# Optimization experiments

Measured on AMD Instinct MI355X. Metric: run time of the kernel, lower is better.

Reference implementation:

```python
import jax, jax.numpy as jnp
import numpy as np

EPS_FP32 = 1e-8
MASK_VALUE = -1.0e9
D_MODEL = 1024
N_HEADS = 16
D_K = D_MODEL // N_HEADS
SCALE = 1.0 / np.sqrt(D_K)


def stable_softmax(x, axis=-1):
    x_max = jnp.max(x, axis=axis, keepdims=True)
    e = jnp.exp(x - x_max)
    return e / (jnp.sum(e, axis=axis, keepdims=True) + EPS_FP32)


def setup_inputs() -> dict:
    key = jax.random.key(0)
    ks = jax.random.split(key, 10)
    B, S, D = 2, 2048, D_MODEL
    x = jax.random.normal(ks[0], (B, S, D), dtype=jnp.float32)
    # causal mask, broadcastable to [B, H, S, S]; 0 -> masked
    mask = jnp.tril(jnp.ones((S, S), dtype=jnp.int32))[None, None, :, :]
    w_scale = 0.02
    Wq = jax.random.normal(ks[1], (D, D), dtype=jnp.float32) * w_scale
    Wk = jax.random.normal(ks[2], (D, D), dtype=jnp.float32) * w_scale
    Wv = jax.random.normal(ks[3], (D, D), dtype=jnp.float32) * w_scale
    Wo = jax.random.normal(ks[4], (D, D), dtype=jnp.float32) * (w_scale * 0.2)
    bq = jnp.zeros((D,), dtype=jnp.float32)
    bk = jnp.zeros((D,), dtype=jnp.float32)
    bv = jnp.zeros((D,), dtype=jnp.float32)
    bo = jnp.zeros((D,), dtype=jnp.float32)
    return {"x": x, "Wq": Wq, "bq": bq, "Wk": Wk, "bk": bk,
            "Wv": Wv, "bv": bv, "Wo": Wo, "bo": bo, "mask": mask}


def reference(x, Wq, bq, Wk, bk, Wv, bv, Wo, bo, mask):
    B, S, D = x.shape
    H, Dk = N_HEADS, D_K
    # torch nn.Linear: y = x @ W.T + b
    def proj(W, b):
        y = jnp.einsum('bsd,ed->bse', x, W) + b
        return y.reshape(B, S, H, Dk).transpose(0, 2, 1, 3)  # [B,H,S,Dk]
    Q = proj(Wq, bq)
    K = proj(Wk, bk)
    V = proj(Wv, bv)
    scores = jnp.einsum('bhqd,bhkd->bhqk', Q, K) * SCALE  # [B,H,S,S]
    scores = jnp.where(mask == 0, MASK_VALUE, scores)
    attn = stable_softmax(scores, axis=-1)
    out = jnp.einsum('bhqk,bhkd->bhqd', attn, V)  # [B,H,S,Dk]
    out = out.transpose(0, 2, 1, 3).reshape(B, S, D)
    return jnp.einsum('bsd,ed->bse', out, Wo) + bo
```

## Files before the change

kernel.cpp:

```cpp
#include <hip/hip_runtime.h>
#include <math.h>

typedef float v4f __attribute__((ext_vector_type(4)));
typedef __bf16 v8y __attribute__((ext_vector_type(8)));
typedef __attribute__((address_space(1))) const void av1_t;
typedef __attribute__((address_space(3))) void av3_t;
typedef unsigned short u16;

#define SCALE_ 0.125f
#define MASKV_ (-1.0e9f)

__device__ __forceinline__ u16 bfhi(float f) {
  union { float f; unsigned u; } v; v.f = f;
  return (u16)(v.u >> 16);
}
__device__ __forceinline__ float bf2f(u16 h) {
  union { unsigned u; float f; } v; v.u = ((unsigned)h) << 16;
  return v.f;
}
__device__ __forceinline__ v4f mfma16(v8y a, v8y b, v4f c) {
  return __builtin_amdgcn_mfma_f32_16x16x32_bf16(a, b, c, 0, 0, 0);
}
__device__ __forceinline__ void gload16(const void* g, void* l) {
  __builtin_amdgcn_global_load_lds((av1_t*)g, (av3_t*)l, 16, 0, 0);
}

__global__ __launch_bounds__(256) void split_kernel(const float* __restrict__ src,
                                                    u16* __restrict__ dst) {
  const int idx = blockIdx.x * 256 + threadIdx.x;
  const int row = idx >> 8, c4 = idx & 255;
  const float4 v = ((const float4*)src)[idx];
  const u16 h0 = bfhi(v.x), h1 = bfhi(v.y), h2 = bfhi(v.z), h3 = bfhi(v.w);
  ushort4 hi, lo;
  hi.x = h0; hi.y = h1; hi.z = h2; hi.w = h3;
  lo.x = bfhi(v.x - bf2f(h0)); lo.y = bfhi(v.y - bf2f(h1));
  lo.z = bfhi(v.z - bf2f(h2)); lo.w = bfhi(v.w - bf2f(h3));
  *(ushort4*)&dst[(size_t)row * 2048 + c4 * 4] = hi;
  *(ushort4*)&dst[(size_t)row * 2048 + 1024 + c4 * 4] = lo;
}

__global__ __launch_bounds__(256) void splitw_kernel(
    const float* __restrict__ Wq, const float* __restrict__ Wk,
    const float* __restrict__ Wv, u16* __restrict__ dst) {
  const int r = blockIdx.x;
  const int c4 = threadIdx.x;
  const float* src = (r < 1024) ? Wq + (size_t)r * 1024
                   : (r < 2048) ? Wk + (size_t)(r - 1024) * 1024
                                : Wv + (size_t)(r - 2048) * 1024;
  const float4 v = ((const float4*)src)[c4];
  const u16 h0 = bfhi(v.x), h1 = bfhi(v.y), h2 = bfhi(v.z), h3 = bfhi(v.w);
  ushort4 hi, lo;
  hi.x = h0; hi.y = h1; hi.z = h2; hi.w = h3;
  lo.x = bfhi(v.x - bf2f(h0)); lo.y = bfhi(v.y - bf2f(h1));
  lo.z = bfhi(v.z - bf2f(h2)); lo.w = bfhi(v.w - bf2f(h3));
  *(ushort4*)&dst[(size_t)r * 2048 + c4 * 4] = hi;
  *(ushort4*)&dst[(size_t)r * 2048 + 1024 + c4 * 4] = lo;
}

__global__ __launch_bounds__(256) void gemm3_kernel(
    const u16* __restrict__ A2, const u16* __restrict__ B2,
    const float* __restrict__ bias0, const float* __restrict__ bias1,
    const float* __restrict__ bias2,
    float* __restrict__ outF,
    u16* __restrict__ Q2, u16* __restrict__ K2,
    u16* __restrict__ Vthi, u16* __restrict__ Vtlo,
    int ntiles_n, int mode)
{
  __shared__ __align__(16) u16 sm[16384];
  char* smc = (char*)sm;
  const int tid = threadIdx.x;
  const int lane = tid & 63;
  const int wid = tid >> 6;
  const int wm = wid >> 1, wn = wid & 1;
  const int l15 = lane & 15, ck = lane >> 4;

  int bid = blockIdx.x;
  const int cpx = gridDim.x >> 3;
  bid = (bid & 7) * cpx + (bid >> 3);
  const int mt = bid / ntiles_n, nt = bid % ntiles_n;
  const int m0 = mt * 128, n0 = nt * 128;

  int offA[4], offB[4];
  #pragma unroll
  for (int i = 0; i < 4; ++i) {
    const int row = wm * 64 + i * 16 + l15;
    offA[i] = row * 64 + (((ck + ((row >> 1) & 3)) & 3) * 16);
  }
  #pragma unroll
  for (int j = 0; j < 4; ++j) {
    const int row = wn * 64 + j * 16 + l15;
    offB[j] = row * 64 + (((ck + ((row >> 1) & 3)) & 3) * 16);
  }

  v4f acc[4][4];
  #pragma unroll
  for (int i = 0; i < 4; ++i)
    #pragma unroll
    for (int j = 0; j < 4; ++j) { v4f z = {0.f, 0.f, 0.f, 0.f}; acc[i][j] = z; }

  #pragma unroll 1
  for (int s = 0; s < 32; ++s) {
    __syncthreads();
    #pragma unroll
    for (int p = 0; p < 8; ++p) {
      const int w = (p & 1) * 256 + tid;
      const int row = w >> 2, cph = w & 3;
      const int clog = (cph - ((row >> 1) & 3)) & 3;
      const int qi = p >> 1;
      const u16* src = (qi < 2) ? A2 : B2;
      const int r0 = (qi < 2) ? m0 : n0;
      const int qoff = (qi & 1) * 1024;
      gload16(&src[(size_t)(r0 + row) * 2048 + qoff + s * 32 + clog * 8],
              smc + p * 4096 + wid * 1024);
    }
    __syncthreads();

    v8y bhi[4], af[4];
    #pragma unroll
    for (int j = 0; j < 4; ++j) bhi[j] = *(const v8y*)(smc + 16384 + offB[j]);

    #pragma unroll
    for (int i = 0; i < 4; ++i) af[i] = *(const v8y*)(smc + offA[i]);
    #pragma unroll
    for (int j = 0; j < 4; ++j)
      #pragma unroll
      for (int i = 0; i < 4; ++i)
        acc[i][j] = mfma16(af[i], bhi[j], acc[i][j]);

    #pragma unroll
    for (int i = 0; i < 4; ++i) af[i] = *(const v8y*)(smc + 8192 + offA[i]);
    #pragma unroll
    for (int j = 0; j < 4; ++j)
      #pragma unroll
      for (int i = 0; i < 4; ++i)
        acc[i][j] = mfma16(af[i], bhi[j], acc[i][j]);

    v8y blo[4];
    #pragma unroll
    for (int j = 0; j < 4; ++j) blo[j] = *(const v8y*)(smc + 24576 + offB[j]);
    #pragma unroll
    for (int i = 0; i < 4; ++i) af[i] = *(const v8y*)(smc + offA[i]);
    #pragma unroll
    for (int j = 0; j < 4; ++j)
      #pragma unroll
      for (int i = 0; i < 4; ++i)
        acc[i][j] = mfma16(af[i], blo[j], acc[i][j]);
  }

  #pragma unroll
  for (int i = 0; i < 4; ++i) {
    #pragma unroll
    for (int j = 0; j < 4; ++j) {
      #pragma unroll
      for (int r = 0; r < 4; ++r) {
        const int m = m0 + wm * 64 + i * 16 + (lane >> 4) * 4 + r;
        const int n = n0 + wn * 64 + j * 16 + (lane & 15);
        float y = acc[i][j][r];
        if (mode == 0) {
          outF[(size_t)m * 1024 + n] = y + bias0[n];
        } else {
          const int which = n >> 10;
          const int nn = n & 1023;
          const int hh = nn >> 6, dk = n & 63;
          const int b = m >> 11, sr = m & 2047;
          y += (which == 0 ? bias0[nn] : (which == 1 ? bias1[nn] : bias2[nn]));
          const u16 hi = bfhi(y);
          const u16 lo = bfhi(y - bf2f(hi));
          const size_t bh = (size_t)(b * 16 + hh);
          if (which == 2) {
            const size_t a = (bh * 64 + dk) * 2048 + sr;
            Vthi[a] = hi; Vtlo[a] = lo;
          } else {
            u16* dst = (which == 0) ? Q2 : K2;
            const size_t a = (bh * 2048 + sr) * 128 + dk;
            dst[a] = hi; dst[a + 64] = lo;
          }
        }
      }
    }
  }
}

__global__ __launch_bounds__(256) void attn_kernel(
    const u16* __restrict__ Q2, const u16* __restrict__ K2,
    const u16* __restrict__ Vthi, const u16* __restrict__ Vtlo,
    u16* __restrict__ ctx2)
{
  __shared__ __align__(16) u16 sm[24576];
  const int tid = threadIdx.x, lane = tid & 63, wid = tid >> 6;
  const int h = blockIdx.y, b = blockIdx.z;
  const size_t bh = (size_t)(b * 16 + h);
  const u16* Qb = Q2 + bh * 2048 * 128;
  const u16* Kb = K2 + bh * 2048 * 128;
  const u16* Vhb = Vthi + bh * (size_t)64 * 2048;
  const u16* Vlb = Vtlo + bh * (size_t)64 * 2048;

  #pragma unroll 1
  for (int half = 0; half < 2; ++half) {
    const int qt = (half == 0) ? (int)blockIdx.x : 31 - (int)blockIdx.x;
    const int q0 = qt * 64;

    v8y qf[4];
    #pragma unroll
    for (int pc = 0; pc < 4; ++pc)
      qf[pc] = *(const v8y*)&Qb[(size_t)(q0 + wid * 16 + (lane & 15)) * 128
                                + pc * 32 + (lane >> 4) * 8];

    v4f o[4];
    float mrun[4], lrun[4];
    #pragma unroll
    for (int nb = 0; nb < 4; ++nb) { v4f z = {0.f,0.f,0.f,0.f}; o[nb] = z; }
    #pragma unroll
    for (int r = 0; r < 4; ++r) { mrun[r] = -INFINITY; lrun[r] = 0.f; }

    for (int kb = 0; kb <= qt; ++kb) {
      const int k0 = kb * 64;
      __syncthreads();
      #pragma unroll
      for (int p = 0; p < 4; ++p) {
        const int u = p * 256 + tid;
        const int row = u >> 4, c = u & 15;
        const int cph = c ^ (row & 7);
        const uint4 kv = *(const uint4*)&Kb[(size_t)(k0 + row) * 128 + c * 8];
        *(uint4*)((char*)sm + row * 256 + cph * 16) = kv;
        const uint4 vv = (c < 8)
            ? *(const uint4*)&Vhb[(size_t)row * 2048 + k0 + c * 8]
            : *(const uint4*)&Vlb[(size_t)row * 2048 + k0 + (c - 8) * 8];
        *(uint4*)((char*)sm + 16384 + row * 256 + cph * 16) = vv;
      }
      __syncthreads();

      v4f s[4];
      #pragma unroll
      for (int nb = 0; nb < 4; ++nb) { v4f z = {0.f,0.f,0.f,0.f}; s[nb] = z; }
      #pragma unroll
      for (int kc = 0; kc < 6; ++kc) {
        const int ma = (kc < 2) ? kc : kc - 2;
        const int mb = (kc < 4) ? kc : kc - 4;
        #pragma unroll
        for (int nb = 0; nb < 4; ++nb) {
          const int row = nb * 16 + (lane & 15);
          const int ch = (mb * 4 + (lane >> 4)) ^ (row & 7);
          const v8y kf = *(const v8y*)((const char*)sm + row * 256 + ch * 16);
          s[nb] = mfma16(qf[ma], kf, s[nb]);
        }
      }

      const bool domask = (kb == qt);
      float alpha[4];
      char* pbase = (char*)sm + 32768 + wid * 4096;
      #pragma unroll
      for (int r = 0; r < 4; ++r) {
        float sv[4];
        #pragma unroll
        for (int nb = 0; nb < 4; ++nb) {
          float v = s[nb][r] * SCALE_;
          if (domask) {
            const int qg = q0 + wid * 16 + (lane >> 4) * 4 + r;
            const int kg = k0 + nb * 16 + (lane & 15);
            if (kg > qg) v = MASKV_;
          }
          sv[nb] = v;
        }
        float rm = fmaxf(fmaxf(sv[0], sv[1]), fmaxf(sv[2], sv[3]));
        rm = fmaxf(rm, __shfl_xor(rm, 1));
        rm = fmaxf(rm, __shfl_xor(rm, 2));
        rm = fmaxf(rm, __shfl_xor(rm, 4));
        rm = fmaxf(rm, __shfl_xor(rm, 8));
        const float mnew = fmaxf(mrun[r], rm);
        const float al = __expf(mrun[r] - mnew);
        const int pr = (lane >> 4) * 4 + r;
        char* prow = pbase + pr * 256;
        float ls = 0.f;
        #pragma unroll
        for (int nb = 0; nb < 4; ++nb) {
          const float pv = __expf(sv[nb] - mnew);
          ls += pv;
          const u16 phi = bfhi(pv);
          const u16 plo = bfhi(pv - bf2f(phi));
          const int kp = nb * 16 + (lane & 15);
          *(u16*)(prow + (((kp >> 3)       ^ (pr & 7)) * 16) + (kp & 7) * 2) = phi;
          *(u16*)(prow + (((8 + (kp >> 3)) ^ (pr & 7)) * 16) + (kp & 7) * 2) = plo;
        }
        ls += __shfl_xor(ls, 1);
        ls += __shfl_xor(ls, 2);
        ls += __shfl_xor(ls, 4);
        ls += __shfl_xor(ls, 8);
        lrun[r] = lrun[r] * al + ls;
        mrun[r] = mnew;
        alpha[r] = al;
      }
      #pragma unroll
      for (int nb = 0; nb < 4; ++nb)
        #pragma unroll
        for (int r = 0; r < 4; ++r)
          o[nb][r] *= alpha[r];

      #pragma unroll
      for (int kc = 0; kc < 6; ++kc) {
        const int ma = (kc < 2) ? kc : kc - 2;
        const int mb = (kc < 4) ? kc : kc - 4;
        const int prow_r = lane & 15;
        const int pch = (ma * 4 + (lane >> 4)) ^ (prow_r & 7);
        const v8y pf = *(const v8y*)(pbase + prow_r * 256 + pch * 16);
        #pragma unroll
        for (int nb = 0; nb < 4; ++nb) {
          const int row = nb * 16 + (lane & 15);
          const int ch = (mb * 4 + (lane >> 4)) ^ (row & 7);
          const v8y vf = *(const v8y*)((const char*)sm + 16384 + row * 256 + ch * 16);
          o[nb] = mfma16(pf, vf, o[nb]);
        }
      }
    }

    #pragma unroll
    for (int r = 0; r < 4; ++r) {
      const float inv = 1.0f / (lrun[r] + 1e-8f);
      const int q = q0 + wid * 16 + (lane >> 4) * 4 + r;
      const size_t mrow = (size_t)(b * 2048 + q) * 2048;
      #pragma unroll
      for (int nb = 0; nb < 4; ++nb) {
        const float y = o[nb][r] * inv;
        const u16 hi = bfhi(y);
        const u16 lo = bfhi(y - bf2f(hi));
        const int col = h * 64 + nb * 16 + (lane & 15);
        ctx2[mrow + col] = hi;
        ctx2[mrow + 1024 + col] = lo;
      }
    }
  }
}

extern "C" void kernel_launch(void* const* d_in, const int* in_sizes, int n_in,
                              void* d_out, int out_size, void* d_ws, size_t ws_size,
                              hipStream_t stream)
{
  const float* x  = (const float*)d_in[0];
  const float* Wq = (const float*)d_in[1];
  const float* bq = (const float*)d_in[2];
  const float* Wk = (const float*)d_in[3];
  const float* bk = (const float*)d_in[4];
  const float* Wv = (const float*)d_in[5];
  const float* bv = (const float*)d_in[6];
  const float* Wo = (const float*)d_in[7];
  const float* bo = (const float*)d_in[8];

  u16* wsp  = (u16*)d_ws;
  u16* Q2   = wsp;
  u16* K2   = Q2 + (size_t)32 * 2048 * 128;
  u16* Vthi = K2 + (size_t)32 * 2048 * 128;
  u16* Vtlo = Vthi + (size_t)32 * 64 * 2048;
  u16* ctx2 = Vtlo + (size_t)32 * 64 * 2048;
  u16* W2   = ctx2;
  u16* Wo2  = Q2;
  u16* X2   = (u16*)d_out;

  split_kernel<<<4096, 256, 0, stream>>>(x, X2);
  splitw_kernel<<<3072, 256, 0, stream>>>(Wq, Wk, Wv, W2);

  gemm3_kernel<<<768, 256, 0, stream>>>(X2, W2, bq, bk, bv,
                                        nullptr, Q2, K2, Vthi, Vtlo, 24, 1);

  attn_kernel<<<dim3(16, 16, 2), 256, 0, stream>>>(Q2, K2, Vthi, Vtlo, ctx2);

  split_kernel<<<1024, 256, 0, stream>>>(Wo, Wo2);

  gemm3_kernel<<<256, 256, 0, stream>>>(ctx2, Wo2, bo, nullptr, nullptr,
                                        (float*)d_out, nullptr, nullptr, nullptr, nullptr,
                                        8, 0);
}
```

Measured before the change: 391.9 us.

## Double-buffer GEMM LDS staging and use smaller M tiles for output projection

The split-bf16 GEMM is templated on its M tile size. LDS is now double-buffered, so the async global-to-LDS loads for the next K step are issued before the MFMAs on the current buffer, leaving one barrier per iteration instead of two. The output projection switches to 64-row tiles, which doubles its grid to 512 blocks for better CU coverage. The cost is double the LDS per block for the QKV GEMM (64KB), which may reduce occupancy.

```diff
diff --git a/kernel.cpp b/kernel.cpp
--- a/kernel.cpp
+++ b/kernel.cpp
@@ -57,7 +57,8 @@
   *(ushort4*)&dst[(size_t)r * 2048 + 1024 + c4 * 4] = lo;
 }
 
-__global__ __launch_bounds__(256) void gemm3_kernel(
+template<int MI>
+__global__ __launch_bounds__(256) void gemm2_kernel(
     const u16* __restrict__ A2, const u16* __restrict__ B2,
     const float* __restrict__ bias0, const float* __restrict__ bias1,
     const float* __restrict__ bias2,
@@ -66,7 +67,9 @@
     u16* __restrict__ Vthi, u16* __restrict__ Vtlo,
     int ntiles_n, int mode)
 {
-  __shared__ __align__(16) u16 sm[16384];
+  constexpr int TM = MI * 32;
+  constexpr int BUFB = TM * 128 + 16384;
+  __shared__ __align__(16) u16 sm[BUFB];
   char* smc = (char*)sm;
   const int tid = threadIdx.x;
   const int lane = tid & 63;
@@ -78,12 +81,12 @@
   const int cpx = gridDim.x >> 3;
   bid = (bid & 7) * cpx + (bid >> 3);
   const int mt = bid / ntiles_n, nt = bid % ntiles_n;
-  const int m0 = mt * 128, n0 = nt * 128;
-
-  int offA[4], offB[4];
+  const int m0 = mt * TM, n0 = nt * 128;
+
+  int offA[MI], offB[4];
   #pragma unroll
-  for (int i = 0; i < 4; ++i) {
-    const int row = wm * 64 + i * 16 + l15;
+  for (int i = 0; i < MI; ++i) {
+    const int row = wm * (MI * 16) + i * 16 + l15;
     offA[i] = row * 64 + (((ck + ((row >> 1) & 3)) & 3) * 16);
   }
   #pragma unroll
@@ -92,68 +95,84 @@
     offB[j] = row * 64 + (((ck + ((row >> 1) & 3)) & 3) * 16);
   }
 
-  v4f acc[4][4];
+  auto STAGE = [&](char* bufc, int s) {
+    #pragma unroll
+    for (int r = 0; r < MI / 2; ++r) {
+      const int w = r * 256 + tid;
+      const int row = w >> 2, cph = w & 3;
+      const int clog = (cph - ((row >> 1) & 3)) & 3;
+      const size_t ga = (size_t)(m0 + row) * 2048 + s * 32 + clog * 8;
+      gload16(&A2[ga], bufc + w * 16);
+      gload16(&A2[ga + 1024], bufc + TM * 64 + w * 16);
+    }
+    #pragma unroll
+    for (int r = 0; r < 2; ++r) {
+      const int w = r * 256 + tid;
+      const int row = w >> 2, cph = w & 3;
+      const int clog = (cph - ((row >> 1) & 3)) & 3;
+      const size_t gb = (size_t)(n0 + row) * 2048 + s * 32 + clog * 8;
+      gload16(&B2[gb], bufc + TM * 128 + w * 16);
+      gload16(&B2[gb + 1024], bufc + TM * 128 + 8192 + w * 16);
+    }
+  };
+
+  v4f acc[MI][4];
   #pragma unroll
-  for (int i = 0; i < 4; ++i)
+  for (int i = 0; i < MI; ++i)
     #pragma unroll
     for (int j = 0; j < 4; ++j) { v4f z = {0.f, 0.f, 0.f, 0.f}; acc[i][j] = z; }
+
+  STAGE(smc, 0);
+  __syncthreads();
+  int cur = 0;
 
   #pragma unroll 1
   for (int s = 0; s < 32; ++s) {
+    char* cb = smc + cur * BUFB;
+    if (s < 31) STAGE(smc + (cur ^ 1) * BUFB, s + 1);
+
+    v8y bhi[4], af[MI];
+    #pragma unroll
+    for (int j = 0; j < 4; ++j) bhi[j] = *(const v8y*)(cb + TM * 128 + offB[j]);
+
+    #pragma unroll
+    for (int i = 0; i < MI; ++i) af[i] = *(const v8y*)(cb + offA[i]);
+    #pragma unroll
+    for (int j = 0; j < 4; ++j)
+      #pragma unroll
+      for (int i = 0; i < MI; ++i)
+        acc[i][j] = mfma16(af[i], bhi[j], acc[i][j]);
+
+    #pragma unroll
+    for (int i = 0; i < MI; ++i) af[i] = *(const v8y*)(cb + TM * 64 + offA[i]);
+    #pragma unroll
+    for (int j = 0; j < 4; ++j)
+      #pragma unroll
+      for (int i = 0; i < MI; ++i)
+        acc[i][j] = mfma16(af[i], bhi[j], acc[i][j]);
+
+    v8y blo[4];
+    #pragma unroll
+    for (int j = 0; j < 4; ++j) blo[j] = *(const v8y*)(cb + TM * 128 + 8192 + offB[j]);
+    #pragma unroll
+    for (int i = 0; i < MI; ++i) af[i] = *(const v8y*)(cb + offA[i]);
+    #pragma unroll
+    for (int j = 0; j < 4; ++j)
+      #pragma unroll
+      for (int i = 0; i < MI; ++i)
+        acc[i][j] = mfma16(af[i], blo[j], acc[i][j]);
+
     __syncthreads();
-    #pragma unroll
-    for (int p = 0; p < 8; ++p) {
-      const int w = (p & 1) * 256 + tid;
-      const int row = w >> 2, cph = w & 3;
-      const int clog = (cph - ((row >> 1) & 3)) & 3;
-      const int qi = p >> 1;
-      const u16* src = (qi < 2) ? A2 : B2;
-      const int r0 = (qi < 2) ? m0 : n0;
-      const int qoff = (qi & 1) * 1024;
-      gload16(&src[(size_t)(r0 + row) * 2048 + qoff + s * 32 + clog * 8],
-              smc + p * 4096 + wid * 1024);
-    }
-    __syncthreads();
-
-    v8y bhi[4], af[4];
-    #pragma unroll
-    for (int j = 0; j < 4; ++j) bhi[j] = *(const v8y*)(smc + 16384 + offB[j]);
-
-    #pragma unroll
-    for (int i = 0; i < 4; ++i) af[i] = *(const v8y*)(smc + offA[i]);
-    #pragma unroll
-    for (int j = 0; j < 4; ++j)
-      #pragma unroll
-      for (int i = 0; i < 4; ++i)
-        acc[i][j] = mfma16(af[i], bhi[j], acc[i][j]);
-
-    #pragma unroll
-    for (int i = 0; i < 4; ++i) af[i] = *(const v8y*)(smc + 8192 + offA[i]);
-    #pragma unroll
-    for (int j = 0; j < 4; ++j)
-      #pragma unroll
-      for (int i = 0; i < 4; ++i)
-        acc[i][j] = mfma16(af[i], bhi[j], acc[i][j]);
-
-    v8y blo[4];
-    #pragma unroll
-    for (int j = 0; j < 4; ++j) blo[j] = *(const v8y*)(smc + 24576 + offB[j]);
-    #pragma unroll
-    for (int i = 0; i < 4; ++i) af[i] = *(const v8y*)(smc + offA[i]);
-    #pragma unroll
-    for (int j = 0; j < 4; ++j)
-      #pragma unroll
-      for (int i = 0; i < 4; ++i)
-        acc[i][j] = mfma16(af[i], blo[j], acc[i][j]);
+    cur ^= 1;
   }
 
   #pragma unroll
-  for (int i = 0; i < 4; ++i) {
+  for (int i = 0; i < MI; ++i) {
     #pragma unroll
     for (int j = 0; j < 4; ++j) {
       #pragma unroll
       for (int r = 0; r < 4; ++r) {
-        const int m = m0 + wm * 64 + i * 16 + (lane >> 4) * 4 + r;
+        const int m = m0 + wm * (MI * 16) + i * 16 + (lane >> 4) * 4 + r;
         const int n = n0 + wn * 64 + j * 16 + (lane & 15);
         float y = acc[i][j][r];
         if (mode == 0) {
@@ -358,14 +377,14 @@
   split_kernel<<<4096, 256, 0, stream>>>(x, X2);
   splitw_kernel<<<3072, 256, 0, stream>>>(Wq, Wk, Wv, W2);
 
-  gemm3_kernel<<<768, 256, 0, stream>>>(X2, W2, bq, bk, bv,
-                                        nullptr, Q2, K2, Vthi, Vtlo, 24, 1);
+  gemm2_kernel<4><<<768, 256, 0, stream>>>(X2, W2, bq, bk, bv,
+                                           nullptr, Q2, K2, Vthi, Vtlo, 24, 1);
 
   attn_kernel<<<dim3(16, 16, 2), 256, 0, stream>>>(Q2, K2, Vthi, Vtlo, ctx2);
 
   split_kernel<<<1024, 256, 0, stream>>>(Wo, Wo2);
 
-  gemm3_kernel<<<256, 256, 0, stream>>>(ctx2, Wo2, bo, nullptr, nullptr,
-                                        (float*)d_out, nullptr, nullptr, nullptr, nullptr,
-                                        8, 0);
-}
+  gemm2_kernel<2><<<512, 256, 0, stream>>>(ctx2, Wo2, bo, nullptr, nullptr,
+                                           (float*)d_out, nullptr, nullptr, nullptr, nullptr,
+                                           8, 0);
+}
```

Result: faster. 374.4 us (-4.5%).
